# Performance work log

Measured on AMD Instinct MI355X. Metric: run time of the kernel, lower is better.

Reference implementation:

```python
import jax, jax.numpy as jnp
import numpy as np

N_NODES = 50000
N_REL = 8
N_EDGES = 400000  # per relation
D_IN = 256
D_OUT = 256


def setup_inputs() -> dict:
    key = jax.random.key(0)
    k1, k2, k3, k4, k5 = jax.random.split(key, 5)
    gain = np.sqrt(2.0)  # relu gain used by xavier init in the module
    x = jax.random.normal(k1, (N_NODES, D_IN), dtype=jnp.float32)
    weight = jax.random.normal(k2, (N_REL, D_IN, D_OUT), dtype=jnp.float32) * (gain / np.sqrt(D_IN + D_OUT))
    h_bias = jnp.zeros((D_OUT,), dtype=jnp.float32)
    loop_weight = jax.random.normal(k3, (D_IN, D_OUT), dtype=jnp.float32) * (gain / np.sqrt(D_IN + D_OUT))
    src_idx = jax.random.randint(k4, (N_REL, N_EDGES), 0, N_NODES, dtype=jnp.int32)
    dst_idx = jax.random.randint(k5, (N_REL, N_EDGES), 0, N_NODES, dtype=jnp.int32)
    return {"x": x, "weight": weight, "h_bias": h_bias, "loop_weight": loop_weight,
            "src_idx": src_idx, "dst_idx": dst_idx}


def reference(x, weight, h_bias, loop_weight, src_idx, dst_idx):
    # x: [N, D_in]; weight: [R, D_in, D_out]; src/dst_idx: [R, E]
    n = x.shape[0]
    out = jnp.zeros((n, weight.shape[-1]), dtype=x.dtype)
    # Loop over the small fixed set of relations (structurally distinct weights).
    for r in range(weight.shape[0]):
        h = x @ weight[r]                                   # [N, D_out] transform-first (in<=out path of GraphConv)
        msg = h[src_idx[r]]                                 # [E, D_out] gather
        agg = jax.ops.segment_sum(msg, dst_idx[r], num_segments=n)  # [N, D_out] scatter-add
        deg = jax.ops.segment_sum(jnp.ones((dst_idx.shape[1],), dtype=x.dtype),
                                  dst_idx[r], num_segments=n)
        out = out + agg / jnp.clip(deg, 1.0)[:, None]       # norm='right': divide by in-degree (clamped at 1)
    out = out + x @ loop_weight + h_bias                    # self-loop + bias
    return jax.nn.relu(out)                                  # activation; dropout(p=0) is identity
```

## Files before the change

### kernel.cpp

```cpp
#include <hip/hip_runtime.h>
#include <hip/hip_bf16.h>

#define NN 50000
#define NPAD 50048
#define NR 8
#define NE 400000
#define CAP 32
#define CHUNK 2048
#define CPB 196
#define NRANGE 6250
#define XBLK 12500
#define TBLK 144

typedef __attribute__((ext_vector_type(8))) short short8v;
typedef __attribute__((ext_vector_type(4))) float f32x4;
typedef __attribute__((ext_vector_type(2))) unsigned int uint2v;

static __device__ __forceinline__ ushort f2b(float f) {
  union { float f; unsigned u; } v; v.f = f;
  unsigned u = v.u;
  unsigned r = (u + 0x7fffu + ((u >> 16) & 1u)) >> 16;
  return (ushort)r;
}
static __device__ __forceinline__ float b2f(ushort u) {
  union { unsigned u; float f; } v; v.u = ((unsigned)u) << 16;
  return v.f;
}


__global__ __launch_bounds__(256) void k_prep(const float* __restrict__ x,
                                              const float* __restrict__ w,
                                              const float* __restrict__ lw,
                                              ushort* __restrict__ xb,
                                              ushort* __restrict__ wb,
                                              const int* __restrict__ src,
                                              const int* __restrict__ dst,
                                              int* __restrict__ cnt,
                                              ushort* __restrict__ csrp) {
  __shared__ ushort tile[64][66];
  int b = blockIdx.x;
  if (b < XBLK) {
    int i = b * 256 + threadIdx.x;
    float4 v = ((const float4*)x)[i];
    ushort4 o;
    o.x = f2b(v.x); o.y = f2b(v.y); o.z = f2b(v.z); o.w = f2b(v.w);
    ((ushort4*)xb)[i] = o;
    return;
  }
  if (b < XBLK + TBLK) {
    int tb = b - XBLK;
    int s = tb >> 4, t16 = tb & 15;
    int kt = (t16 >> 2) * 64, nt2 = (t16 & 3) * 64;
    const float* srcw = (s < 8) ? (w + (size_t)s * 65536) : lw;
    int t = threadIdx.x;
    #pragma unroll
    for (int i = 0; i < 16; ++i) {
      int flat = i * 256 + t;
      int kk = flat >> 6, nn = flat & 63;
      tile[kk][nn] = f2b(srcw[(size_t)(kt + kk) * 256 + nt2 + nn]);
    }
    __syncthreads();
    #pragma unroll
    for (int i = 0; i < 16; ++i) {
      int flat = i * 256 + t;
      int nn2 = flat >> 6, kk2 = flat & 63;
      wb[(size_t)s * 65536 + (size_t)(nt2 + nn2) * 256 + kt + kk2] = tile[kk2][nn2];
    }
    return;
  }
  int xcd = b & 7;
  int rc = (b - XBLK - TBLK) >> 3;
  int r = rc / CPB;
  int c = rc - r * CPB;
  int nlo = xcd * NRANGE, nhi = nlo + NRANGE;
  const int* dr = dst + (size_t)r * NE;
  const int* sr = src + (size_t)r * NE;
  int e0 = c * CHUNK + threadIdx.x * 4;
  #pragma unroll
  for (int u = 0; u < CHUNK / 1024; ++u) {
    int e = e0 + u * 1024;
    if (e + 3 < NE) {
      int4 d4 = *(const int4*)(dr + e);
      int4 s4 = *(const int4*)(sr + e);
      #pragma unroll
      for (int k = 0; k < 4; ++k) {
        int d = (k == 0) ? d4.x : (k == 1) ? d4.y : (k == 2) ? d4.z : d4.w;
        int s = (k == 0) ? s4.x : (k == 1) ? s4.y : (k == 2) ? s4.z : s4.w;
        if (d >= nlo && d < nhi) {
          int slot = atomicAdd(&cnt[r * NN + d], 1);
          if (slot < CAP)
            csrp[((size_t)r * NN + d) * CAP + slot] = (ushort)s;
        }
      }
    } else {
      for (int k = 0; k < 4; ++k) {
        int e2 = e + k;
        if (e2 < NE) {
          int d = dr[e2];
          if (d >= nlo && d < nhi) {
            int slot = atomicAdd(&cnt[r * NN + d], 1);
            if (slot < CAP)
              csrp[((size_t)r * NN + d) * CAP + slot] = (ushort)sr[e2];
          }
        }
      }
    }
  }
}


__global__ __launch_bounds__(256) void k_agg(const ushort* __restrict__ xb,
                                             const ushort* __restrict__ csrp,
                                             const int* __restrict__ cnt,
                                             ushort* __restrict__ xa,
                                             long strideR, int r0) {
  int wid = threadIdx.x >> 6, lane = threadIdx.x & 63;
  int n = blockIdx.x * 4 + wid;
  int r = r0 + blockIdx.y;
  if (n >= NN) return;
  int dg = cnt[r * NN + n];
  int m = min(dg, CAP);
  const ushort* lst = csrp + ((size_t)r * NN + n) * CAP;
  float a0 = 0.f, a1 = 0.f, a2 = 0.f, a3 = 0.f;
  int j = 0;
  for (; j + 3 < m; j += 4) {
    int s0 = lst[j], s1 = lst[j + 1], s2 = lst[j + 2], s3 = lst[j + 3];
    ushort4 v0 = *(const ushort4*)(xb + (size_t)s0 * 256 + lane * 4);
    ushort4 v1 = *(const ushort4*)(xb + (size_t)s1 * 256 + lane * 4);
    ushort4 v2 = *(const ushort4*)(xb + (size_t)s2 * 256 + lane * 4);
    ushort4 v3 = *(const ushort4*)(xb + (size_t)s3 * 256 + lane * 4);
    a0 += (b2f(v0.x) + b2f(v1.x)) + (b2f(v2.x) + b2f(v3.x));
    a1 += (b2f(v0.y) + b2f(v1.y)) + (b2f(v2.y) + b2f(v3.y));
    a2 += (b2f(v0.z) + b2f(v1.z)) + (b2f(v2.z) + b2f(v3.z));
    a3 += (b2f(v0.w) + b2f(v1.w)) + (b2f(v2.w) + b2f(v3.w));
  }
  for (; j < m; ++j) {
    ushort4 v0 = *(const ushort4*)(xb + (size_t)lst[j] * 256 + lane * 4);
    a0 += b2f(v0.x); a1 += b2f(v0.y); a2 += b2f(v0.z); a3 += b2f(v0.w);
  }
  float inv = 1.f / (float)max(dg, 1);
  unsigned w0 = ((unsigned)f2b(a0 * inv)) | (((unsigned)f2b(a1 * inv)) << 16);
  unsigned w1 = ((unsigned)f2b(a2 * inv)) | (((unsigned)f2b(a3 * inv)) << 16);
  uint2v o; o[0] = w0; o[1] = w1;
  __builtin_nontemporal_store(o, (uint2v*)(xa + (size_t)(r - r0) * strideR +
                                           (size_t)n * 256 + lane * 4));
}


#define BK 64

__global__ __launch_bounds__(512, 4) void k_gemm(
    const ushort* __restrict__ xa, long strideR, int nseg,
    const ushort* __restrict__ xb8, const ushort* __restrict__ wb, int wseg0,
    const float* __restrict__ bias, float* __restrict__ out, int first, int final_) {
  __shared__ ushort As[128 * BK];
  __shared__ ushort Bs[256 * BK];
  int t = threadIdx.x;
  int lane = t & 63, wid = t >> 6;
  int wm = wid >> 2, wn = wid & 3;
  int i0 = blockIdx.x * 128;

  f32x4 acc[4][4];
  #pragma unroll
  for (int a = 0; a < 4; ++a)
    #pragma unroll
    for (int b = 0; b < 4; ++b) acc[a][b] = (f32x4){0.f, 0.f, 0.f, 0.f};

  for (int s = 0; s < nseg; ++s) {
    const ushort* A = (wseg0 + s < 8) ? (xa + (size_t)s * strideR) : xb8;
    const ushort* W = wb + (size_t)(wseg0 + s) * 65536;
    for (int kt = 0; kt < 256; kt += BK) {
      __syncthreads();
      #pragma unroll
      for (int it = 0; it < 2; ++it) {
        int c = it * 512 + t;
        int row = c >> 3, sg = c & 7;
        int sgg = sg ^ (row & 7);
        const ushort* ga = A + (size_t)(i0 + row) * 256 + kt + sgg * 8;
        __builtin_amdgcn_global_load_lds(
            (const __attribute__((address_space(1))) unsigned int*)ga,
            (__attribute__((address_space(3))) unsigned int*)(As + c * 8), 16, 0, 0);
      }
      #pragma unroll
      for (int it = 0; it < 4; ++it) {
        int c = it * 512 + t;
        int row = c >> 3, sg = c & 7;
        int sgg = sg ^ (row & 7);
        const ushort* gb = W + (size_t)row * 256 + kt + sgg * 8;
        __builtin_amdgcn_global_load_lds(
            (const __attribute__((address_space(1))) unsigned int*)gb,
            (__attribute__((address_space(3))) unsigned int*)(Bs + c * 8), 16, 0, 0);
      }
      __syncthreads();
      #pragma unroll
      for (int kk = 0; kk < 2; ++kk) {
        int ko = kk * 32 + (lane >> 4) * 8;
        int kb = ko * 2;
        short8v a_frag[4], b_frag[4];
        #pragma unroll
        for (int mi = 0; mi < 4; ++mi) {
          int row = wm * 64 + mi * 16 + (lane & 15);
          int ba = row * 128 + (kb ^ ((row & 7) << 4));
          a_frag[mi] = *(const short8v*)((const char*)As + ba);
        }
        #pragma unroll
        for (int ni = 0; ni < 4; ++ni) {
          int row = wn * 64 + ni * 16 + (lane & 15);
          int ba = row * 128 + (kb ^ ((row & 7) << 4));
          b_frag[ni] = *(const short8v*)((const char*)Bs + ba);
        }
        #pragma unroll
        for (int mi = 0; mi < 4; ++mi)
          #pragma unroll
          for (int ni = 0; ni < 4; ++ni)
            acc[mi][ni] = __builtin_amdgcn_mfma_f32_16x16x32_bf16(
                a_frag[mi], b_frag[ni], acc[mi][ni], 0, 0, 0);
      }
    }
  }

  #pragma unroll
  for (int mi = 0; mi < 4; ++mi) {
    int rbase = i0 + wm * 64 + mi * 16 + ((lane >> 4) << 2);
    #pragma unroll
    for (int ni = 0; ni < 4; ++ni) {
      int col = wn * 64 + ni * 16 + (lane & 15);
      float bv = final_ ? bias[col] : 0.f;
      #pragma unroll
      for (int rg = 0; rg < 4; ++rg) {
        int gm = rbase + rg;
        if (gm < NN) {
          size_t o = (size_t)gm * 256 + col;
          float v = acc[mi][ni][rg];
          if (!first) v += out[o];
          if (final_) v = fmaxf(v + bv, 0.f);
          out[o] = v;
        }
      }
    }
  }
}


extern "C" void kernel_launch(void* const* d_in, const int* in_sizes, int n_in,
                              void* d_out, int out_size, void* d_ws, size_t ws_size,
                              hipStream_t stream) {
  const float* x = (const float*)d_in[0];
  const float* w = (const float*)d_in[1];
  const float* bias = (const float*)d_in[2];
  const float* lw = (const float*)d_in[3];
  const int* src = (const int*)d_in[4];
  const int* dst = (const int*)d_in[5];
  float* out = (float*)d_out;

  char* ws = (char*)d_ws;
  size_t off = 0;
  auto carve = [&](size_t bytes) {
    size_t o = off;
    off = (off + bytes + 255) & ~(size_t)255;
    return o;
  };
  int* cnt = (int*)(ws + carve((size_t)NR * NN * 4));
  ushort* csrp = (ushort*)(ws + carve((size_t)NR * NN * CAP * 2));
  ushort* wb = (ushort*)(ws + carve((size_t)9 * 65536 * 2));
  ushort* xb = (ushort*)(ws + carve((size_t)NPAD * 256 * 2));
  size_t base_bytes = off;
  ushort* xa = (ushort*)(ws + off);
  const size_t segb = (size_t)NPAD * 256 * 2;
  long strideR = (long)NPAD * 256;

  (void)hipMemsetAsync(cnt, 0, (size_t)NR * NN * 4, stream);
  k_prep<<<XBLK + TBLK + 8 * CPB * NR, 256, 0, stream>>>(x, w, lw, xb, wb,
                                                         src, dst, cnt, csrp);

  dim3 gemm_grid(NPAD / 128);
  if (ws_size >= base_bytes + 8 * segb) {
    k_agg<<<dim3((NN + 3) / 4, 8), 256, 0, stream>>>(xb, csrp, cnt, xa, strideR, 0);
    k_gemm<<<gemm_grid, 512, 0, stream>>>(xa, strideR, 9, xb, wb, 0, bias, out, 1, 1);
  } else if (ws_size >= base_bytes + 4 * segb) {
    k_agg<<<dim3((NN + 3) / 4, 4), 256, 0, stream>>>(xb, csrp, cnt, xa, strideR, 0);
    k_gemm<<<gemm_grid, 512, 0, stream>>>(xa, strideR, 4, xb, wb, 0, bias, out, 1, 0);
    k_agg<<<dim3((NN + 3) / 4, 4), 256, 0, stream>>>(xb, csrp, cnt, xa, strideR, 4);
    k_gemm<<<gemm_grid, 512, 0, stream>>>(xa, strideR, 5, xb, wb, 4, bias, out, 0, 1);
  } else {
    for (int r = 0; r < 8; ++r) {
      k_agg<<<dim3((NN + 3) / 4, 1), 256, 0, stream>>>(xb, csrp, cnt, xa, strideR, r);
      k_gemm<<<gemm_grid, 512, 0, stream>>>(xa, strideR, 1, xb, wb, r, bias, out,
                                            (r == 0) ? 1 : 0, 0);
    }
    k_gemm<<<gemm_grid, 512, 0, stream>>>(xa, strideR, 1, xb, wb, 8, bias, out, 0, 1);
  }
  (void)in_sizes; (void)n_in; (void)out_size;
}
```

Measured before the change: 464.5 us.

## Double-buffer A tile in GEMM to prefetch next k-step during compute

Splits the A-operand LDS tile into two buffers and flattens the segment/k loops into a single step loop. The next step's A tile is issued via global_load_lds before waiting on the current step, with vmcnt(2) used to wait only for the current loads. The goal is to overlap part of the global-to-LDS traffic with MFMA compute. It adds LDS usage, which may reduce occupancy, and B is still single-buffered, so the overlap is partial.

Measured after the change: 453.6 us. -2.3%, faster.

```diff
diff --git a/kernel.cpp b/kernel.cpp
--- a/kernel.cpp
+++ b/kernel.cpp
@@ -153,12 +153,13 @@
     const ushort* __restrict__ xa, long strideR, int nseg,
     const ushort* __restrict__ xb8, const ushort* __restrict__ wb, int wseg0,
     const float* __restrict__ bias, float* __restrict__ out, int first, int final_) {
-  __shared__ ushort As[128 * BK];
+  __shared__ ushort As[2][128 * BK];
   __shared__ ushort Bs[256 * BK];
   int t = threadIdx.x;
   int lane = t & 63, wid = t >> 6;
   int wm = wid >> 2, wn = wid & 3;
   int i0 = blockIdx.x * 128;
+  const int NT = nseg * 4;
 
   f32x4 acc[4][4];
   #pragma unroll
@@ -166,58 +167,78 @@
     #pragma unroll
     for (int b = 0; b < 4; ++b) acc[a][b] = (f32x4){0.f, 0.f, 0.f, 0.f};
 
-  for (int s = 0; s < nseg; ++s) {
-    const ushort* A = (wseg0 + s < 8) ? (xa + (size_t)s * strideR) : xb8;
-    const ushort* W = wb + (size_t)(wseg0 + s) * 65536;
-    for (int kt = 0; kt < 256; kt += BK) {
-      __syncthreads();
-      #pragma unroll
-      for (int it = 0; it < 2; ++it) {
-        int c = it * 512 + t;
-        int row = c >> 3, sg = c & 7;
-        int sgg = sg ^ (row & 7);
-        const ushort* ga = A + (size_t)(i0 + row) * 256 + kt + sgg * 8;
-        __builtin_amdgcn_global_load_lds(
-            (const __attribute__((address_space(1))) unsigned int*)ga,
-            (__attribute__((address_space(3))) unsigned int*)(As + c * 8), 16, 0, 0);
-      }
-      #pragma unroll
-      for (int it = 0; it < 4; ++it) {
-        int c = it * 512 + t;
-        int row = c >> 3, sg = c & 7;
-        int sgg = sg ^ (row & 7);
-        const ushort* gb = W + (size_t)row * 256 + kt + sgg * 8;
-        __builtin_amdgcn_global_load_lds(
-            (const __attribute__((address_space(1))) unsigned int*)gb,
-            (__attribute__((address_space(3))) unsigned int*)(Bs + c * 8), 16, 0, 0);
-      }
-      __syncthreads();
-      #pragma unroll
-      for (int kk = 0; kk < 2; ++kk) {
-        int ko = kk * 32 + (lane >> 4) * 8;
-        int kb = ko * 2;
-        short8v a_frag[4], b_frag[4];
+#define STAGE_A(stp, buf) do {                                                  \
+    int s_ = (stp) >> 2; int kt_ = ((stp) & 3) * 64;                            \
+    const ushort* A_ = (wseg0 + s_ < 8) ? (xa + (size_t)s_ * strideR) : xb8;    \
+    _Pragma("unroll")                                                           \
+    for (int it = 0; it < 2; ++it) {                                            \
+      int c = it * 512 + t; int row = c >> 3, sg = c & 7;                       \
+      int sgg = sg ^ (row & 7);                                                 \
+      const ushort* ga = A_ + (size_t)(i0 + row) * 256 + kt_ + sgg * 8;         \
+      __builtin_amdgcn_global_load_lds(                                         \
+          (const __attribute__((address_space(1))) unsigned int*)ga,            \
+          (__attribute__((address_space(3))) unsigned int*)(As[buf] + c * 8),   \
+          16, 0, 0);                                                            \
+    } } while (0)
+
+#define STAGE_B(stp) do {                                                       \
+    int s_ = (stp) >> 2; int kt_ = ((stp) & 3) * 64;                            \
+    const ushort* W_ = wb + (size_t)(wseg0 + s_) * 65536;                       \
+    _Pragma("unroll")                                                           \
+    for (int it = 0; it < 4; ++it) {                                            \
+      int c = it * 512 + t; int row = c >> 3, sg = c & 7;                       \
+      int sgg = sg ^ (row & 7);                                                 \
+      const ushort* gb = W_ + (size_t)row * 256 + kt_ + sgg * 8;                \
+      __builtin_amdgcn_global_load_lds(                                         \
+          (const __attribute__((address_space(1))) unsigned int*)gb,            \
+          (__attribute__((address_space(3))) unsigned int*)(Bs + c * 8),        \
+          16, 0, 0);                                                            \
+    } } while (0)
+
+  STAGE_A(0, 0);
+  int cur = 0;
+  #pragma unroll 1
+  for (int st = 0; st < NT; ++st) {
+    __builtin_amdgcn_s_barrier();
+    STAGE_B(st);
+    if (st + 1 < NT) {
+      STAGE_A(st + 1, cur ^ 1);
+      asm volatile("s_waitcnt vmcnt(2)" ::: "memory");
+    } else {
+      asm volatile("s_waitcnt vmcnt(0)" ::: "memory");
+    }
+    __builtin_amdgcn_sched_barrier(0);
+    __builtin_amdgcn_s_barrier();
+    __builtin_amdgcn_sched_barrier(0);
+    const ushort* Ac = As[cur];
+    #pragma unroll
+    for (int kk = 0; kk < 2; ++kk) {
+      int ko = kk * 32 + (lane >> 4) * 8;
+      int kb = ko * 2;
+      short8v a_frag[4], b_frag[4];
+      #pragma unroll
+      for (int mi = 0; mi < 4; ++mi) {
+        int row = wm * 64 + mi * 16 + (lane & 15);
+        int ba = row * 128 + (kb ^ ((row & 7) << 4));
+        a_frag[mi] = *(const short8v*)((const char*)Ac + ba);
+      }
+      #pragma unroll
+      for (int ni = 0; ni < 4; ++ni) {
+        int row = wn * 64 + ni * 16 + (lane & 15);
+        int ba = row * 128 + (kb ^ ((row & 7) << 4));
+        b_frag[ni] = *(const short8v*)((const char*)Bs + ba);
+      }
+      #pragma unroll
+      for (int mi = 0; mi < 4; ++mi)
         #pragma unroll
-        for (int mi = 0; mi < 4; ++mi) {
-          int row = wm * 64 + mi * 16 + (lane & 15);
-          int ba = row * 128 + (kb ^ ((row & 7) << 4));
-          a_frag[mi] = *(const short8v*)((const char*)As + ba);
-        }
-        #pragma unroll
-        for (int ni = 0; ni < 4; ++ni) {
-          int row = wn * 64 + ni * 16 + (lane & 15);
-          int ba = row * 128 + (kb ^ ((row & 7) << 4));
-          b_frag[ni] = *(const short8v*)((const char*)Bs + ba);
-        }
-        #pragma unroll
-        for (int mi = 0; mi < 4; ++mi)
-          #pragma unroll
-          for (int ni = 0; ni < 4; ++ni)
-            acc[mi][ni] = __builtin_amdgcn_mfma_f32_16x16x32_bf16(
-                a_frag[mi], b_frag[ni], acc[mi][ni], 0, 0, 0);
-      }
-    }
-  }
+        for (int ni = 0; ni < 4; ++ni)
+          acc[mi][ni] = __builtin_amdgcn_mfma_f32_16x16x32_bf16(
+              a_frag[mi], b_frag[ni], acc[mi][ni], 0, 0, 0);
+    }
+    cur ^= 1;
+  }
+#undef STAGE_A
+#undef STAGE_B
 
   #pragma unroll
   for (int mi = 0; mi < 4; ++mi) {
```

## Fuse neighbor aggregation into the relation GEMM kernel via shared-memory A tiles

Applied to the files above, without the earlier changes.

Replaces the separate aggregation kernel and GEMM kernel with a single fused kernel. Each block aggregates neighbor features for its 64 nodes per relation directly into an LDS A tile, then multiplies by that relation's weight, accumulating across all 9 segments in registers. This removes the intermediate aggregated-feature buffer round-trip through HBM and the extra kernel launch. In exchange the GEMM tile shrinks to 64 rows, occupancy drops to 2 blocks, and the gather latency is serialized with the MFMA phase inside each block instead of overlapping across kernels.

After: 552.3 us. +18.9%, slower.

```diff
diff --git a/kernel.cpp b/kernel.cpp
--- a/kernel.cpp
+++ b/kernel.cpp
@@ -109,84 +109,100 @@
 }
 
 
-__global__ __launch_bounds__(256) void k_agg(const ushort* __restrict__ xb,
-                                             const ushort* __restrict__ csrp,
-                                             const int* __restrict__ cnt,
-                                             ushort* __restrict__ xa,
-                                             long strideR, int r0) {
-  int wid = threadIdx.x >> 6, lane = threadIdx.x & 63;
-  int n = blockIdx.x * 4 + wid;
-  int r = r0 + blockIdx.y;
-  if (n >= NN) return;
-  int dg = cnt[r * NN + n];
-  int m = min(dg, CAP);
-  const ushort* lst = csrp + ((size_t)r * NN + n) * CAP;
-  float a0 = 0.f, a1 = 0.f, a2 = 0.f, a3 = 0.f;
-  int j = 0;
-  for (; j + 3 < m; j += 4) {
-    int s0 = lst[j], s1 = lst[j + 1], s2 = lst[j + 2], s3 = lst[j + 3];
-    ushort4 v0 = *(const ushort4*)(xb + (size_t)s0 * 256 + lane * 4);
-    ushort4 v1 = *(const ushort4*)(xb + (size_t)s1 * 256 + lane * 4);
-    ushort4 v2 = *(const ushort4*)(xb + (size_t)s2 * 256 + lane * 4);
-    ushort4 v3 = *(const ushort4*)(xb + (size_t)s3 * 256 + lane * 4);
-    a0 += (b2f(v0.x) + b2f(v1.x)) + (b2f(v2.x) + b2f(v3.x));
-    a1 += (b2f(v0.y) + b2f(v1.y)) + (b2f(v2.y) + b2f(v3.y));
-    a2 += (b2f(v0.z) + b2f(v1.z)) + (b2f(v2.z) + b2f(v3.z));
-    a3 += (b2f(v0.w) + b2f(v1.w)) + (b2f(v2.w) + b2f(v3.w));
-  }
-  for (; j < m; ++j) {
-    ushort4 v0 = *(const ushort4*)(xb + (size_t)lst[j] * 256 + lane * 4);
-    a0 += b2f(v0.x); a1 += b2f(v0.y); a2 += b2f(v0.z); a3 += b2f(v0.w);
-  }
-  float inv = 1.f / (float)max(dg, 1);
-  unsigned w0 = ((unsigned)f2b(a0 * inv)) | (((unsigned)f2b(a1 * inv)) << 16);
-  unsigned w1 = ((unsigned)f2b(a2 * inv)) | (((unsigned)f2b(a3 * inv)) << 16);
-  uint2v o; o[0] = w0; o[1] = w1;
-  __builtin_nontemporal_store(o, (uint2v*)(xa + (size_t)(r - r0) * strideR +
-                                           (size_t)n * 256 + lane * 4));
-}
-
-
-#define BK 64
-
-__global__ __launch_bounds__(512, 4) void k_gemm(
-    const ushort* __restrict__ xa, long strideR, int nseg,
-    const ushort* __restrict__ xb8, const ushort* __restrict__ wb, int wseg0,
-    const float* __restrict__ bias, float* __restrict__ out, int first, int final_) {
-  __shared__ ushort As[128 * BK];
-  __shared__ ushort Bs[256 * BK];
-  int t = threadIdx.x;
-  int lane = t & 63, wid = t >> 6;
+__global__ __launch_bounds__(512, 2) void k_fused(
+    const ushort* __restrict__ xb, const ushort* __restrict__ wb,
+    const ushort* __restrict__ csrp, const int* __restrict__ cnt,
+    const float* __restrict__ bias, float* __restrict__ out) {
+  __shared__ ushort As[64 * 256];
+  __shared__ ushort Bs[256 * 64];
+  int t = threadIdx.x, lane = t & 63, wid = t >> 6;
   int wm = wid >> 2, wn = wid & 3;
-  int i0 = blockIdx.x * 128;
-
-  f32x4 acc[4][4];
+  int nb = blockIdx.x * 64;
+
+  f32x4 acc[2][4];
   #pragma unroll
-  for (int a = 0; a < 4; ++a)
+  for (int a = 0; a < 2; ++a)
     #pragma unroll
     for (int b = 0; b < 4; ++b) acc[a][b] = (f32x4){0.f, 0.f, 0.f, 0.f};
 
-  for (int s = 0; s < nseg; ++s) {
-    const ushort* A = (wseg0 + s < 8) ? (xa + (size_t)s * strideR) : xb8;
-    const ushort* W = wb + (size_t)(wseg0 + s) * 65536;
-    for (int kt = 0; kt < 256; kt += BK) {
-      __syncthreads();
-      #pragma unroll
-      for (int it = 0; it < 2; ++it) {
-        int c = it * 512 + t;
-        int row = c >> 3, sg = c & 7;
-        int sgg = sg ^ (row & 7);
-        const ushort* ga = A + (size_t)(i0 + row) * 256 + kt + sgg * 8;
-        __builtin_amdgcn_global_load_lds(
-            (const __attribute__((address_space(1))) unsigned int*)ga,
-            (__attribute__((address_space(3))) unsigned int*)(As + c * 8), 16, 0, 0);
-      }
+  for (int s = 0; s < 9; ++s) {
+    #pragma unroll 1
+    for (int i = 0; i < 8; ++i) {
+      int row = wid * 8 + i;
+      int n = nb + row;
+      unsigned wbyte = (unsigned)row * 512 + (((unsigned)lane * 8u) ^ (((unsigned)row & 7u) << 4));
+      uint2v o; o[0] = 0u; o[1] = 0u;
+      if (n < NN) {
+        if (s == 8) {
+          o = *(const uint2v*)(xb + (size_t)n * 256 + lane * 4);
+        } else {
+          int dg = cnt[s * NN + n];
+          int m = min(dg, CAP);
+          const ushort* lst = csrp + ((size_t)s * NN + n) * CAP;
+          float a0 = 0.f, a1 = 0.f, a2 = 0.f, a3 = 0.f;
+          int j = 0;
+          for (; j + 8 <= m; j += 8) {
+            int s0 = lst[j], s1 = lst[j+1], s2 = lst[j+2], s3 = lst[j+3];
+            int s4 = lst[j+4], s5 = lst[j+5], s6 = lst[j+6], s7 = lst[j+7];
+            ushort4 v0 = *(const ushort4*)(xb + (size_t)s0 * 256 + lane * 4);
+            ushort4 v1 = *(const ushort4*)(xb + (size_t)s1 * 256 + lane * 4);
+            ushort4 v2 = *(const ushort4*)(xb + (size_t)s2 * 256 + lane * 4);
+            ushort4 v3 = *(const ushort4*)(xb + (size_t)s3 * 256 + lane * 4);
+            ushort4 v4 = *(const ushort4*)(xb + (size_t)s4 * 256 + lane * 4);
+            ushort4 v5 = *(const ushort4*)(xb + (size_t)s5 * 256 + lane * 4);
+            ushort4 v6 = *(const ushort4*)(xb + (size_t)s6 * 256 + lane * 4);
+            ushort4 v7 = *(const ushort4*)(xb + (size_t)s7 * 256 + lane * 4);
+            a0 += ((b2f(v0.x)+b2f(v1.x))+(b2f(v2.x)+b2f(v3.x)))
+                + ((b2f(v4.x)+b2f(v5.x))+(b2f(v6.x)+b2f(v7.x)));
+            a1 += ((b2f(v0.y)+b2f(v1.y))+(b2f(v2.y)+b2f(v3.y)))
+                + ((b2f(v4.y)+b2f(v5.y))+(b2f(v6.y)+b2f(v7.y)));
+            a2 += ((b2f(v0.z)+b2f(v1.z))+(b2f(v2.z)+b2f(v3.z)))
+                + ((b2f(v4.z)+b2f(v5.z))+(b2f(v6.z)+b2f(v7.z)));
+            a3 += ((b2f(v0.w)+b2f(v1.w))+(b2f(v2.w)+b2f(v3.w)))
+                + ((b2f(v4.w)+b2f(v5.w))+(b2f(v6.w)+b2f(v7.w)));
+          }
+          if (m & 4) {
+            int s0 = lst[j], s1 = lst[j+1], s2 = lst[j+2], s3 = lst[j+3];
+            ushort4 v0 = *(const ushort4*)(xb + (size_t)s0 * 256 + lane * 4);
+            ushort4 v1 = *(const ushort4*)(xb + (size_t)s1 * 256 + lane * 4);
+            ushort4 v2 = *(const ushort4*)(xb + (size_t)s2 * 256 + lane * 4);
+            ushort4 v3 = *(const ushort4*)(xb + (size_t)s3 * 256 + lane * 4);
+            a0 += (b2f(v0.x)+b2f(v1.x))+(b2f(v2.x)+b2f(v3.x));
+            a1 += (b2f(v0.y)+b2f(v1.y))+(b2f(v2.y)+b2f(v3.y));
+            a2 += (b2f(v0.z)+b2f(v1.z))+(b2f(v2.z)+b2f(v3.z));
+            a3 += (b2f(v0.w)+b2f(v1.w))+(b2f(v2.w)+b2f(v3.w));
+            j += 4;
+          }
+          if (m & 2) {
+            int s0 = lst[j], s1 = lst[j+1];
+            ushort4 v0 = *(const ushort4*)(xb + (size_t)s0 * 256 + lane * 4);
+            ushort4 v1 = *(const ushort4*)(xb + (size_t)s1 * 256 + lane * 4);
+            a0 += b2f(v0.x)+b2f(v1.x); a1 += b2f(v0.y)+b2f(v1.y);
+            a2 += b2f(v0.z)+b2f(v1.z); a3 += b2f(v0.w)+b2f(v1.w);
+            j += 2;
+          }
+          if (m & 1) {
+            ushort4 v0 = *(const ushort4*)(xb + (size_t)lst[j] * 256 + lane * 4);
+            a0 += b2f(v0.x); a1 += b2f(v0.y); a2 += b2f(v0.z); a3 += b2f(v0.w);
+          }
+          float inv = 1.f / (float)max(dg, 1);
+          o[0] = ((unsigned)f2b(a0 * inv)) | (((unsigned)f2b(a1 * inv)) << 16);
+          o[1] = ((unsigned)f2b(a2 * inv)) | (((unsigned)f2b(a3 * inv)) << 16);
+        }
+      }
+      *(uint2v*)((char*)As + wbyte) = o;
+    }
+    __syncthreads();
+
+    const ushort* W = wb + (size_t)s * 65536;
+    #pragma unroll 1
+    for (int kt = 0; kt < 4; ++kt) {
       #pragma unroll
       for (int it = 0; it < 4; ++it) {
         int c = it * 512 + t;
         int row = c >> 3, sg = c & 7;
         int sgg = sg ^ (row & 7);
-        const ushort* gb = W + (size_t)row * 256 + kt + sgg * 8;
+        const ushort* gb = W + (size_t)row * 256 + kt * 64 + sgg * 8;
         __builtin_amdgcn_global_load_lds(
             (const __attribute__((address_space(1))) unsigned int*)gb,
             (__attribute__((address_space(3))) unsigned int*)(Bs + c * 8), 16, 0, 0);
@@ -195,46 +211,45 @@
       #pragma unroll
       for (int kk = 0; kk < 2; ++kk) {
         int ko = kk * 32 + (lane >> 4) * 8;
-        int kb = ko * 2;
-        short8v a_frag[4], b_frag[4];
+        int kbB = ko * 2;
+        int kbA = (kt * 64 + ko) * 2;
+        short8v a_frag[2], b_frag[4];
         #pragma unroll
-        for (int mi = 0; mi < 4; ++mi) {
-          int row = wm * 64 + mi * 16 + (lane & 15);
-          int ba = row * 128 + (kb ^ ((row & 7) << 4));
+        for (int mi = 0; mi < 2; ++mi) {
+          int row = wm * 32 + mi * 16 + (lane & 15);
+          int ba = row * 512 + (kbA ^ ((row & 7) << 4));
           a_frag[mi] = *(const short8v*)((const char*)As + ba);
         }
         #pragma unroll
         for (int ni = 0; ni < 4; ++ni) {
           int row = wn * 64 + ni * 16 + (lane & 15);
-          int ba = row * 128 + (kb ^ ((row & 7) << 4));
-          b_frag[ni] = *(const short8v*)((const char*)Bs + ba);
+          int bb = row * 128 + (kbB ^ ((row & 7) << 4));
+          b_frag[ni] = *(const short8v*)((const char*)Bs + bb);
         }
         #pragma unroll
-        for (int mi = 0; mi < 4; ++mi)
+        for (int mi = 0; mi < 2; ++mi)
           #pragma unroll
           for (int ni = 0; ni < 4; ++ni)
             acc[mi][ni] = __builtin_amdgcn_mfma_f32_16x16x32_bf16(
                 a_frag[mi], b_frag[ni], acc[mi][ni], 0, 0, 0);
       }
+      __syncthreads();
     }
   }
 
   #pragma unroll
-  for (int mi = 0; mi < 4; ++mi) {
-    int rbase = i0 + wm * 64 + mi * 16 + ((lane >> 4) << 2);
+  for (int mi = 0; mi < 2; ++mi) {
+    int rbase = nb + wm * 32 + mi * 16 + ((lane >> 4) << 2);
     #pragma unroll
     for (int ni = 0; ni < 4; ++ni) {
       int col = wn * 64 + ni * 16 + (lane & 15);
-      float bv = final_ ? bias[col] : 0.f;
+      float bv = bias[col];
       #pragma unroll
       for (int rg = 0; rg < 4; ++rg) {
         int gm = rbase + rg;
         if (gm < NN) {
-          size_t o = (size_t)gm * 256 + col;
-          float v = acc[mi][ni][rg];
-          if (!first) v += out[o];
-          if (final_) v = fmaxf(v + bv, 0.f);
-          out[o] = v;
+          float v = fmaxf(acc[mi][ni][rg] + bv, 0.f);
+          __builtin_nontemporal_store(v, &out[(size_t)gm * 256 + col]);
         }
       }
     }
@@ -264,31 +279,11 @@
   ushort* csrp = (ushort*)(ws + carve((size_t)NR * NN * CAP * 2));
   ushort* wb = (ushort*)(ws + carve((size_t)9 * 65536 * 2));
   ushort* xb = (ushort*)(ws + carve((size_t)NPAD * 256 * 2));
-  size_t base_bytes = off;
-  ushort* xa = (ushort*)(ws + off);
-  const size_t segb = (size_t)NPAD * 256 * 2;
-  long strideR = (long)NPAD * 256;
 
   (void)hipMemsetAsync(cnt, 0, (size_t)NR * NN * 4, stream);
   k_prep<<<XBLK + TBLK + 8 * CPB * NR, 256, 0, stream>>>(x, w, lw, xb, wb,
                                                          src, dst, cnt, csrp);
-
-  dim3 gemm_grid(NPAD / 128);
-  if (ws_size >= base_bytes + 8 * segb) {
-    k_agg<<<dim3((NN + 3) / 4, 8), 256, 0, stream>>>(xb, csrp, cnt, xa, strideR, 0);
-    k_gemm<<<gemm_grid, 512, 0, stream>>>(xa, strideR, 9, xb, wb, 0, bias, out, 1, 1);
-  } else if (ws_size >= base_bytes + 4 * segb) {
-    k_agg<<<dim3((NN + 3) / 4, 4), 256, 0, stream>>>(xb, csrp, cnt, xa, strideR, 0);
-    k_gemm<<<gemm_grid, 512, 0, stream>>>(xa, strideR, 4, xb, wb, 0, bias, out, 1, 0);
-    k_agg<<<dim3((NN + 3) / 4, 4), 256, 0, stream>>>(xb, csrp, cnt, xa, strideR, 4);
-    k_gemm<<<gemm_grid, 512, 0, stream>>>(xa, strideR, 5, xb, wb, 4, bias, out, 0, 1);
-  } else {
-    for (int r = 0; r < 8; ++r) {
-      k_agg<<<dim3((NN + 3) / 4, 1), 256, 0, stream>>>(xb, csrp, cnt, xa, strideR, r);
-      k_gemm<<<gemm_grid, 512, 0, stream>>>(xa, strideR, 1, xb, wb, r, bias, out,
-                                            (r == 0) ? 1 : 0, 0);
-    }
-    k_gemm<<<gemm_grid, 512, 0, stream>>>(xa, strideR, 1, xb, wb, 8, bias, out, 0, 1);
-  }
-  (void)in_sizes; (void)n_in; (void)out_size;
-}
+  k_fused<<<NPAD / 64, 512, 0, stream>>>(xb, wb, csrp, cnt, bias, out);
+
+  (void)in_sizes; (void)n_in; (void)out_size; (void)ws_size;
+}
```
